# Kernel tuning notes

Hardware: AMD Instinct MI355X
Metric: run time of the kernel (lower is better)

## Reference

```python
import jax, jax.numpy as jnp
import numpy as np

B, T, C = 2, 2048, 1024
H = 16
D = C // H  # head_dim = 64


def setup_inputs() -> dict:
    key = jax.random.key(0)
    k1, k2, k3, k4, k5 = jax.random.split(key, 5)
    s = 0.02
    return {
        "x": jax.random.normal(k1, (B, T, C), dtype=jnp.float32),
        "w_qkv": jax.random.normal(k2, (C, 3 * C), dtype=jnp.float32) * s,
        "b_qkv": jnp.zeros((3 * C,), dtype=jnp.float32),
        "w_proj": jax.random.normal(k3, (C, C), dtype=jnp.float32) * s,
        "b_proj": jnp.zeros((C,), dtype=jnp.float32),
    }


def reference(x, w_qkv, b_qkv, w_proj, b_proj):
    b, t, c = x.shape
    qkv = x @ w_qkv + b_qkv                      # [B,T,3C]
    q, k, v = jnp.split(qkv, 3, axis=-1)
    # [B,T,C] -> [B,H,T,D]
    q = q.reshape(b, t, H, D).transpose(0, 2, 1, 3)
    k = k.reshape(b, t, H, D).transpose(0, 2, 1, 3)
    v = v.reshape(b, t, H, D).transpose(0, 2, 1, 3)
    att = jnp.einsum("bhqd,bhkd->bhqk", q, k) / jnp.sqrt(jnp.float32(D))
    causal = jnp.tril(jnp.ones((t, t), dtype=bool))  # True where allowed
    att = jnp.where(causal, att, -jnp.inf)
    att = jax.nn.softmax(att, axis=-1)
    out = jnp.einsum("bhqk,bhkd->bhqd", att, v)      # [B,H,T,D]
    out = out.transpose(0, 2, 1, 3).reshape(b, t, c)
    return out @ w_proj + b_proj
```

## Files before the change

kernel.cpp:

```cpp
#include <hip/hip_runtime.h>
#include <hip/hip_bf16.h>
#include <math.h>
#include <stdint.h>

#define B_ 2
#define T_ 2048
#define C_ 1024
#define H_ 16
#define D_ 64

typedef __attribute__((ext_vector_type(8))) short bf16x8;
typedef __attribute__((ext_vector_type(4))) float f32x4;

__device__ inline short f2bf(float f) {
  __hip_bfloat16 h = __float2bfloat16(f);
  return *(short*)&h;
}

__device__ inline void async16(const void* g, void* l) {
  __builtin_amdgcn_global_load_lds(
      (const __attribute__((address_space(1))) uint32_t*)g,
      (__attribute__((address_space(3))) uint32_t*)l, 16, 0, 0);
}


__global__ __launch_bounds__(256) void convert_x(const float* __restrict__ X,
                                                 short* __restrict__ Xb) {
  int t = blockIdx.x * 256 + threadIdx.x;
  int m = t >> 5, g = t & 31;
  const float* src = X + (size_t)m * C_ + g * 32;
  short* dst = Xb + (size_t)m * C_ + g * 32;
  int xv = (m >> 1) & 3;
  short out[32];
#pragma unroll
  for (int ch = 0; ch < 4; ++ch) {
    int sc = ch ^ xv;
#pragma unroll
    for (int e = 0; e < 8; e += 4) {
      float4 v = *(const float4*)(src + sc * 8 + e);
      out[ch * 8 + e + 0] = f2bf(v.x);
      out[ch * 8 + e + 1] = f2bf(v.y);
      out[ch * 8 + e + 2] = f2bf(v.z);
      out[ch * 8 + e + 3] = f2bf(v.w);
    }
  }
#pragma unroll
  for (int q = 0; q < 4; ++q) *(uint4*)(dst + q * 8) = *(uint4*)(out + q * 8);
}

__global__ __launch_bounds__(256) void transpose_w(const float* __restrict__ W,
                                                   short* __restrict__ Wt,
                                                   int N) {
  const int k0 = blockIdx.y * 64;
  const int n0 = blockIdx.x * 64;
  __shared__ short Ts[64][68];
  const int tid = threadIdx.x;
  {
    int r = tid >> 2, c0 = (tid & 3) * 16;
    const float* src = W + (size_t)(k0 + r) * N + n0 + c0;
#pragma unroll
    for (int u = 0; u < 16; u += 4) {
      float4 v = *(const float4*)(src + u);
      Ts[r][c0 + u + 0] = f2bf(v.x);
      Ts[r][c0 + u + 1] = f2bf(v.y);
      Ts[r][c0 + u + 2] = f2bf(v.z);
      Ts[r][c0 + u + 3] = f2bf(v.w);
    }
  }
  __syncthreads();
  {
    int n = tid >> 2, kb = (tid & 3) * 16;
    int xv = ((n0 + n) >> 1) & 3;
    short* orow = Wt + (size_t)(n0 + n) * 1024 + k0;
#pragma unroll
    for (int cc = 0; cc < 2; ++cc) {
      int ka = kb + cc * 8;
      int dk = (ka & ~31) | ((((ka >> 3) & 3) ^ xv) << 3);
      short tmp[8];
#pragma unroll
      for (int u = 0; u < 8; ++u) tmp[u] = Ts[ka + u][n];
      *(uint4*)(orow + dk) = *(uint4*)tmp;
    }
  }
}

template <int N, bool QKV>
__global__ __launch_bounds__(256) void gemm_mfma(
    const short* __restrict__ A, const short* __restrict__ Bt,
    const float* __restrict__ bias, short* __restrict__ Qp,
    short* __restrict__ Kp, short* __restrict__ Vp, float* __restrict__ Cout) {
  const int tid = threadIdx.x;
  const int wave = tid >> 6, lane = tid & 63;
  const int quad = lane >> 4, l16 = lane & 15;
  const int wm = wave >> 1, wn = wave & 1;
  const int m0 = blockIdx.y * 128, n0 = blockIdx.x * 128;

  __shared__ short As[128 * 32];
  __shared__ short Bs[128 * 32];

  const int srow = tid >> 2, skc = tid & 3;
  const size_t arow0 = (size_t)(m0 + srow) * 1024 + skc * 8;
  const size_t brow0 = (size_t)(n0 + srow) * 1024 + skc * 8;

  f32x4 acc[4][4] = {};

  const int xi = quad ^ ((l16 >> 1) & 3);
  int aoff[4], boff[4];
#pragma unroll
  for (int i = 0; i < 4; ++i) {
    aoff[i] = (wm * 64 + i * 16 + l16) * 32 + xi * 8;
    boff[i] = (wn * 64 + i * 16 + l16) * 32 + xi * 8;
  }

  for (int k0 = 0; k0 < 1024; k0 += 32) {
    __syncthreads();
    async16(A + arow0 + k0, As + tid * 8);
    async16(A + arow0 + (size_t)64 * 1024 + k0, As + 2048 + tid * 8);
    async16(Bt + brow0 + k0, Bs + tid * 8);
    async16(Bt + brow0 + (size_t)64 * 1024 + k0, Bs + 2048 + tid * 8);
    __syncthreads();

    bf16x8 af[4], bfr[4];
#pragma unroll
    for (int i = 0; i < 4; ++i) af[i] = *(const bf16x8*)(As + aoff[i]);
#pragma unroll
    for (int j = 0; j < 4; ++j) bfr[j] = *(const bf16x8*)(Bs + boff[j]);
#pragma unroll
    for (int i = 0; i < 4; ++i)
#pragma unroll
      for (int j = 0; j < 4; ++j)
        acc[i][j] = __builtin_amdgcn_mfma_f32_16x16x32_bf16(af[i], bfr[j],
                                                            acc[i][j], 0, 0, 0);
  }

  float bj[4];
#pragma unroll
  for (int j = 0; j < 4; ++j) bj[j] = bias[n0 + wn * 64 + j * 16 + l16];

  if (QKV) {
#pragma unroll
    for (int i = 0; i < 4; ++i) {
#pragma unroll
      for (int reg = 0; reg < 4; ++reg) {
        int m = m0 + wm * 64 + i * 16 + quad * 4 + reg;
        int b = m >> 11, t = m & (T_ - 1);
#pragma unroll
        for (int j = 0; j < 4; ++j) {
          int n = n0 + wn * 64 + j * 16 + l16;
          float v = acc[i][j][reg] + bj[j];
          int sel = n >> 10, cc = n & (C_ - 1);
          int hh = cc >> 6, d = cc & 63;
          size_t base = (size_t)(b * H_ + hh) * 131072 + (size_t)(t >> 6) * 4096;
          if (sel == 0) {
            Qp[base + (d >> 3) * 512 + (t & 63) * 8 + (d & 7)] = f2bf(v * 0.125f);
          } else if (sel == 1) {
            Kp[base + (d >> 3) * 512 + (t & 63) * 8 + (d & 7)] = f2bf(v);
          } else {
            Vp[base + ((t & 63) >> 3) * 512 + d * 8 + (t & 7)] = f2bf(v);
          }
        }
      }
    }
  } else {
#pragma unroll
    for (int i = 0; i < 4; ++i) {
#pragma unroll
      for (int reg = 0; reg < 4; ++reg) {
        int m = m0 + wm * 64 + i * 16 + quad * 4 + reg;
#pragma unroll
        for (int j = 0; j < 4; ++j) {
          int n = n0 + wn * 64 + j * 16 + l16;
          Cout[(size_t)m * N + n] = acc[i][j][reg] + bj[j];
        }
      }
    }
  }
}

__global__ __launch_bounds__(256, 4) void attn_kernel(
    const short* __restrict__ Qt, const short* __restrict__ Kt,
    const short* __restrict__ Vt, short* __restrict__ attb) {
  const int tid = threadIdx.x;
  const int wave = tid >> 6, lane = tid & 63;
  const int quad = lane >> 4, l16 = lane & 15;

  const int blk = blockIdx.x;
  const int bh = (blk >> 5) & 31;
  const int k2 = blk >> 8;
  int qtt = ((blk & 31) + 8 * (k2 >> 1)) & 31;
  const int qt = (k2 & 1) ? (31 - qtt) : qtt;
  const int h = bh & 15, b = bh >> 4;
  const int q0 = qt * 64;

  const short* Qg = Qt + (size_t)bh * 131072;
  const short* Kg = Kt + (size_t)bh * 131072;
  const short* Vg = Vt + (size_t)bh * 131072;

  __shared__ short Ks[2][4096];
  __shared__ short Vs[2][4096];
  __shared__ short Ps[4096];

  const int rowl = 16 * wave + l16;

  bf16x8 bq[2];
#pragma unroll
  for (int f = 0; f < 2; ++f)
    bq[f] = *(const bf16x8*)(Qg + (size_t)(qt * 8 + 4 * f + quad) * 512 +
                             rowl * 8);

  async16(Kg + tid * 8, &Ks[0][tid * 8]);
  async16(Kg + 2048 + tid * 8, &Ks[0][2048 + tid * 8]);
  async16(Vg + tid * 8, &Vs[0][tid * 8]);
  async16(Vg + 2048 + tid * 8, &Vs[0][2048 + tid * 8]);

  f32x4 oacc[4] = {};
  float lsum = 0.f;

  for (int kt = 0; kt <= qt; ++kt) {
    const int buf = kt & 1;
    __syncthreads();
    if (kt < qt) {
      const short* kp = Kg + (size_t)(kt + 1) * 4096;
      const short* vp = Vg + (size_t)(kt + 1) * 4096;
      async16(kp + tid * 8, &Ks[buf ^ 1][tid * 8]);
      async16(kp + 2048 + tid * 8, &Ks[buf ^ 1][2048 + tid * 8]);
      async16(vp + tid * 8, &Vs[buf ^ 1][tid * 8]);
      async16(vp + 2048 + tid * 8, &Vs[buf ^ 1][2048 + tid * 8]);
    }

    f32x4 sacc[4] = {};
#pragma unroll
    for (int c = 0; c < 4; ++c) {
#pragma unroll
      for (int f = 0; f < 2; ++f) {
        bf16x8 ak = *(const bf16x8*)&Ks[buf][((4 * f + quad) * 64 + 16 * c + l16) * 8];
        sacc[c] = __builtin_amdgcn_mfma_f32_16x16x32_bf16(ak, bq[f], sacc[c], 0, 0, 0);
      }
    }

    const bool diag = (kt == qt);
#pragma unroll
    for (int c = 0; c < 4; ++c) {
      short4 pk;
#pragma unroll
      for (int reg = 0; reg < 4; ++reg) {
        int keyl = 16 * c + 4 * quad + reg;
        float p = (diag && keyl > rowl) ? 0.f : __expf(sacc[c][reg]);
        lsum += p;
        ((short*)&pk)[reg] = f2bf(p);
      }
      *(short4*)&Ps[(2 * c + (quad >> 1)) * 512 + rowl * 8 + (quad & 1) * 4] = pk;
    }

    __asm__ volatile("s_waitcnt lgkmcnt(0)" ::: "memory");

    bf16x8 ap[2];
#pragma unroll
    for (int f = 0; f < 2; ++f)
      ap[f] = *(const bf16x8*)&Ps[(4 * f + quad) * 512 + rowl * 8];
#pragma unroll
    for (int n = 0; n < 4; ++n) {
#pragma unroll
      for (int f = 0; f < 2; ++f) {
        bf16x8 bv = *(const bf16x8*)&Vs[buf][((4 * f + quad) * 64 + 16 * n + l16) * 8];
        oacc[n] = __builtin_amdgcn_mfma_f32_16x16x32_bf16(ap[f], bv, oacc[n], 0, 0, 0);
      }
    }
  }

  lsum += __shfl_xor(lsum, 16);
  lsum += __shfl_xor(lsum, 32);
  float linv[4];
#pragma unroll
  for (int reg = 0; reg < 4; ++reg)
    linv[reg] = 1.0f / __shfl(lsum, 4 * quad + reg, 64);

#pragma unroll
  for (int reg = 0; reg < 4; ++reg) {
    const int row = q0 + 16 * wave + 4 * quad + reg;
    const int m = b * T_ + row;
    const int xv = (m >> 1) & 3;
#pragma unroll
    for (int n = 0; n < 4; ++n) {
      int c = h * 64 + 16 * n + l16;
      int cs = (c & ~31) | ((((c >> 3) & 3) ^ xv) << 3) | (c & 7);
      attb[(size_t)m * C_ + cs] = f2bf(oacc[n][reg] * linv[reg]);
    }
  }
}

extern "C" void kernel_launch(void* const* d_in, const int* in_sizes, int n_in,
                              void* d_out, int out_size, void* d_ws, size_t ws_size,
                              hipStream_t stream) {
  const float* x      = (const float*)d_in[0];
  const float* w_qkv  = (const float*)d_in[1];
  const float* b_qkv  = (const float*)d_in[2];
  const float* w_proj = (const float*)d_in[3];
  const float* b_proj = (const float*)d_in[4];
  float* out = (float*)d_out;

  const size_t per = (size_t)B_ * H_ * T_ * D_;
  short* Qp   = (short*)d_ws;
  short* Kp   = Qp + per;
  short* Vp   = Kp + per;
  short* attb = Vp + per;
  short* xb   = attb + per;
  short* wqt  = xb + per;
  short* wpt  = wqt + (size_t)3 * C_ * C_;

  convert_x<<<512, 256, 0, stream>>>(x, xb);
  transpose_w<<<dim3(48, 16), 256, 0, stream>>>(w_qkv, wqt, 3 * C_);
  transpose_w<<<dim3(16, 16), 256, 0, stream>>>(w_proj, wpt, C_);

  gemm_mfma<3 * C_, true><<<dim3(24, 32), 256, 0, stream>>>(
      xb, wqt, b_qkv, Qp, Kp, Vp, nullptr);

  attn_kernel<<<dim3(1024), 256, 0, stream>>>(Qp, Kp, Vp, attb);

  gemm_mfma<C_, false><<<dim3(8, 32), 256, 0, stream>>>(
      attb, wpt, b_proj, nullptr, nullptr, nullptr, out);
}
```

Baseline: 191.5 us.

## Fuse prep kernels, double-buffer GEMM LDS, narrow proj tile for more blocks

Merges the x conversion and both weight transposes into one launch, and changes the transpose write pattern so each thread writes one 16-byte chunk per pass. The GEMM now double-buffers its LDS tiles, issuing the async load of the next k-slice before computing the current one, which removes one barrier per iteration. The output projection switches to a 64-wide N tile, doubling its grid to fill more CUs. These changes trade more LDS per block and a small branching prep kernel for fewer launches and better latency hiding.

```diff
diff --git a/kernel.cpp b/kernel.cpp
--- a/kernel.cpp
+++ b/kernel.cpp
@@ -24,37 +24,50 @@
 }
 
 
-__global__ __launch_bounds__(256) void convert_x(const float* __restrict__ X,
-                                                 short* __restrict__ Xb) {
-  int t = blockIdx.x * 256 + threadIdx.x;
-  int m = t >> 5, g = t & 31;
-  const float* src = X + (size_t)m * C_ + g * 32;
-  short* dst = Xb + (size_t)m * C_ + g * 32;
-  int xv = (m >> 1) & 3;
-  short out[32];
-#pragma unroll
-  for (int ch = 0; ch < 4; ++ch) {
-    int sc = ch ^ xv;
-#pragma unroll
-    for (int e = 0; e < 8; e += 4) {
-      float4 v = *(const float4*)(src + sc * 8 + e);
-      out[ch * 8 + e + 0] = f2bf(v.x);
-      out[ch * 8 + e + 1] = f2bf(v.y);
-      out[ch * 8 + e + 2] = f2bf(v.z);
-      out[ch * 8 + e + 3] = f2bf(v.w);
-    }
-  }
-#pragma unroll
-  for (int q = 0; q < 4; ++q) *(uint4*)(dst + q * 8) = *(uint4*)(out + q * 8);
-}
-
-__global__ __launch_bounds__(256) void transpose_w(const float* __restrict__ W,
-                                                   short* __restrict__ Wt,
-                                                   int N) {
-  const int k0 = blockIdx.y * 64;
-  const int n0 = blockIdx.x * 64;
+__global__ __launch_bounds__(256) void prep(
+    const float* __restrict__ X, const float* __restrict__ Wq,
+    const float* __restrict__ Wp, short* __restrict__ Xb,
+    short* __restrict__ Wqt, short* __restrict__ Wpt) {
+  const int tid = threadIdx.x;
+  const int blk = blockIdx.x;
   __shared__ short Ts[64][68];
-  const int tid = threadIdx.x;
+
+  if (blk < 512) {
+    int t = blk * 256 + tid;
+    int m = t >> 5, g = t & 31;
+    const float* src = X + (size_t)m * C_ + g * 32;
+    short* dst = Xb + (size_t)m * C_ + g * 32;
+    int xv = (m >> 1) & 3;
+    short out[32];
+#pragma unroll
+    for (int ch = 0; ch < 4; ++ch) {
+      int sc = ch ^ xv;
+#pragma unroll
+      for (int e = 0; e < 8; e += 4) {
+        float4 v = *(const float4*)(src + sc * 8 + e);
+        out[ch * 8 + e + 0] = f2bf(v.x);
+        out[ch * 8 + e + 1] = f2bf(v.y);
+        out[ch * 8 + e + 2] = f2bf(v.z);
+        out[ch * 8 + e + 3] = f2bf(v.w);
+      }
+    }
+#pragma unroll
+    for (int q = 0; q < 4; ++q) *(uint4*)(dst + q * 8) = *(uint4*)(out + q * 8);
+    return;
+  }
+
+  const float* W;
+  short* Wt;
+  int N, n0, k0;
+  if (blk < 1280) {
+    int i = blk - 512;
+    W = Wq; Wt = Wqt; N = 3 * C_;
+    n0 = (i % 48) * 64; k0 = (i / 48) * 64;
+  } else {
+    int i = blk - 1280;
+    W = Wp; Wt = Wpt; N = C_;
+    n0 = (i & 15) * 64; k0 = (i >> 4) * 64;
+  }
   {
     int r = tid >> 2, c0 = (tid & 3) * 16;
     const float* src = W + (size_t)(k0 + r) * N + n0 + c0;
@@ -68,74 +81,79 @@
     }
   }
   __syncthreads();
-  {
-    int n = tid >> 2, kb = (tid & 3) * 16;
+#pragma unroll
+  for (int p = 0; p < 2; ++p) {
+    int n = (tid >> 3) + p * 32;
+    int kc = tid & 7;
     int xv = ((n0 + n) >> 1) & 3;
-    short* orow = Wt + (size_t)(n0 + n) * 1024 + k0;
-#pragma unroll
-    for (int cc = 0; cc < 2; ++cc) {
-      int ka = kb + cc * 8;
-      int dk = (ka & ~31) | ((((ka >> 3) & 3) ^ xv) << 3);
-      short tmp[8];
-#pragma unroll
-      for (int u = 0; u < 8; ++u) tmp[u] = Ts[ka + u][n];
-      *(uint4*)(orow + dk) = *(uint4*)tmp;
-    }
-  }
-}
-
-template <int N, bool QKV>
+    int ka = kc * 8;
+    int dk = (ka & ~31) | ((((ka >> 3) & 3) ^ xv) << 3);
+    short tmp[8];
+#pragma unroll
+    for (int u = 0; u < 8; ++u) tmp[u] = Ts[ka + u][n];
+    *(uint4*)(Wt + (size_t)(n0 + n) * 1024 + k0 + dk) = *(uint4*)tmp;
+  }
+}
+
+template <int N, int BN, bool QKV>
 __global__ __launch_bounds__(256) void gemm_mfma(
     const short* __restrict__ A, const short* __restrict__ Bt,
     const float* __restrict__ bias, short* __restrict__ Qp,
     short* __restrict__ Kp, short* __restrict__ Vp, float* __restrict__ Cout) {
+  constexpr int NJ = BN / 32;
   const int tid = threadIdx.x;
   const int wave = tid >> 6, lane = tid & 63;
   const int quad = lane >> 4, l16 = lane & 15;
   const int wm = wave >> 1, wn = wave & 1;
-  const int m0 = blockIdx.y * 128, n0 = blockIdx.x * 128;
-
-  __shared__ short As[128 * 32];
-  __shared__ short Bs[128 * 32];
+  const int m0 = blockIdx.y * 128, n0 = blockIdx.x * BN;
+
+  __shared__ short As[2][4096];
+  __shared__ short Bs[2][BN * 32];
 
   const int srow = tid >> 2, skc = tid & 3;
   const size_t arow0 = (size_t)(m0 + srow) * 1024 + skc * 8;
   const size_t brow0 = (size_t)(n0 + srow) * 1024 + skc * 8;
 
-  f32x4 acc[4][4] = {};
+  f32x4 acc[4][NJ] = {};
 
   const int xi = quad ^ ((l16 >> 1) & 3);
-  int aoff[4], boff[4];
-#pragma unroll
-  for (int i = 0; i < 4; ++i) {
-    aoff[i] = (wm * 64 + i * 16 + l16) * 32 + xi * 8;
-    boff[i] = (wn * 64 + i * 16 + l16) * 32 + xi * 8;
-  }
-
-  for (int k0 = 0; k0 < 1024; k0 += 32) {
+  int aoff[4], boff[NJ];
+#pragma unroll
+  for (int i = 0; i < 4; ++i) aoff[i] = (wm * 64 + i * 16 + l16) * 32 + xi * 8;
+#pragma unroll
+  for (int j = 0; j < NJ; ++j)
+    boff[j] = (wn * (BN / 2) + j * 16 + l16) * 32 + xi * 8;
+
+  auto stage = [&](int k0, int buf) {
+    async16(A + arow0 + k0, &As[buf][tid * 8]);
+    async16(A + arow0 + (size_t)64 * 1024 + k0, &As[buf][2048 + tid * 8]);
+    async16(Bt + brow0 + k0, &Bs[buf][tid * 8]);
+    if (BN == 128)
+      async16(Bt + brow0 + (size_t)64 * 1024 + k0, &Bs[buf][2048 + tid * 8]);
+  };
+
+  stage(0, 0);
+  for (int kt = 0; kt < 32; ++kt) {
+    const int buf = kt & 1;
     __syncthreads();
-    async16(A + arow0 + k0, As + tid * 8);
-    async16(A + arow0 + (size_t)64 * 1024 + k0, As + 2048 + tid * 8);
-    async16(Bt + brow0 + k0, Bs + tid * 8);
-    async16(Bt + brow0 + (size_t)64 * 1024 + k0, Bs + 2048 + tid * 8);
-    __syncthreads();
-
-    bf16x8 af[4], bfr[4];
-#pragma unroll
-    for (int i = 0; i < 4; ++i) af[i] = *(const bf16x8*)(As + aoff[i]);
-#pragma unroll
-    for (int j = 0; j < 4; ++j) bfr[j] = *(const bf16x8*)(Bs + boff[j]);
+    if (kt < 31) stage((kt + 1) * 32, buf ^ 1);
+
+    bf16x8 af[4], bfr[NJ];
+#pragma unroll
+    for (int i = 0; i < 4; ++i) af[i] = *(const bf16x8*)&As[buf][aoff[i]];
+#pragma unroll
+    for (int j = 0; j < NJ; ++j) bfr[j] = *(const bf16x8*)&Bs[buf][boff[j]];
 #pragma unroll
     for (int i = 0; i < 4; ++i)
 #pragma unroll
-      for (int j = 0; j < 4; ++j)
+      for (int j = 0; j < NJ; ++j)
         acc[i][j] = __builtin_amdgcn_mfma_f32_16x16x32_bf16(af[i], bfr[j],
                                                             acc[i][j], 0, 0, 0);
   }
 
-  float bj[4];
-#pragma unroll
-  for (int j = 0; j < 4; ++j) bj[j] = bias[n0 + wn * 64 + j * 16 + l16];
+  float bj[NJ];
+#pragma unroll
+  for (int j = 0; j < NJ; ++j) bj[j] = bias[n0 + wn * (BN / 2) + j * 16 + l16];
 
   if (QKV) {
 #pragma unroll
@@ -145,8 +163,8 @@
         int m = m0 + wm * 64 + i * 16 + quad * 4 + reg;
         int b = m >> 11, t = m & (T_ - 1);
 #pragma unroll
-        for (int j = 0; j < 4; ++j) {
-          int n = n0 + wn * 64 + j * 16 + l16;
+        for (int j = 0; j < NJ; ++j) {
+          int n = n0 + wn * (BN / 2) + j * 16 + l16;
           float v = acc[i][j][reg] + bj[j];
           int sel = n >> 10, cc = n & (C_ - 1);
           int hh = cc >> 6, d = cc & 63;
@@ -168,8 +186,8 @@
       for (int reg = 0; reg < 4; ++reg) {
         int m = m0 + wm * 64 + i * 16 + quad * 4 + reg;
 #pragma unroll
-        for (int j = 0; j < 4; ++j) {
-          int n = n0 + wn * 64 + j * 16 + l16;
+        for (int j = 0; j < NJ; ++j) {
+          int n = n0 + wn * (BN / 2) + j * 16 + l16;
           Cout[(size_t)m * N + n] = acc[i][j][reg] + bj[j];
         }
       }
@@ -308,15 +326,13 @@
   short* wqt  = xb + per;
   short* wpt  = wqt + (size_t)3 * C_ * C_;
 
-  convert_x<<<512, 256, 0, stream>>>(x, xb);
-  transpose_w<<<dim3(48, 16), 256, 0, stream>>>(w_qkv, wqt, 3 * C_);
-  transpose_w<<<dim3(16, 16), 256, 0, stream>>>(w_proj, wpt, C_);
-
-  gemm_mfma<3 * C_, true><<<dim3(24, 32), 256, 0, stream>>>(
+  prep<<<1536, 256, 0, stream>>>(x, w_qkv, w_proj, xb, wqt, wpt);
+
+  gemm_mfma<3 * C_, 128, true><<<dim3(24, 32), 256, 0, stream>>>(
       xb, wqt, b_qkv, Qp, Kp, Vp, nullptr);
 
   attn_kernel<<<dim3(1024), 256, 0, stream>>>(Qp, Kp, Vp, attb);
 
-  gemm_mfma<C_, false><<<dim3(8, 32), 256, 0, stream>>>(
+  gemm_mfma<C_, 64, false><<<dim3(16, 32), 256, 0, stream>>>(
       attb, wpt, b_proj, nullptr, nullptr, nullptr, out);
 }
```

Measured after the change: 189.9 us. About the same (-0.9%).
